# Kernel tuning notes

Measured on AMD Instinct MI355X. Metric: run time of the kernel, lower is better.

Reference implementation:

```python
import jax, jax.numpy as jnp
import numpy as np

K = 30           # SortPooling k (init kwarg)
B = 8192         # number of graphs in batch
MAX_N = 96       # max nodes per graph (sizes lie in [32, 96])
D = 128          # total_dim (feature width)


def _make_spans():
    # Ragged graph sizes in [32, 96], built in complementary pairs (a, 128-a)
    # so the total node count is exactly B * 64.
    i = np.arange(B // 2)
    a = 32 + (i * 7919) % 65          # in [32, 96]
    sizes = np.empty(B, dtype=np.int64)
    sizes[0::2] = a
    sizes[1::2] = 128 - a
    ends = np.cumsum(sizes)
    starts = ends - sizes
    return np.stack([starts, ends], axis=1)  # [B, 2]


def setup_inputs() -> dict:
    key = jax.random.key(0)
    spans = _make_spans()
    n_total = int(spans[-1, 1])  # 524288
    features = jax.random.normal(key, (n_total, D), dtype=jnp.float32)
    graph_indexes = jnp.asarray(spans, dtype=jnp.int64)
    return {"features": features, "graph_indexes": graph_indexes}


def reference(features, graph_indexes):
    n_total = features.shape[0]
    starts = graph_indexes[:, 0]                      # [B]
    ends = graph_indexes[:, 1]                        # [B]
    # Dense window per graph: indices start..start+MAX_N, masked past the end.
    idx = starts[:, None] + jnp.arange(MAX_N, dtype=graph_indexes.dtype)[None, :]  # [B, MAX_N]
    valid = idx < ends[:, None]                       # [B, MAX_N]
    g = features[jnp.minimum(idx, n_total - 1)]       # [B, MAX_N, D]
    # Sort key = last feature column; invalid slots -> -inf so they lose.
    sort_key = jnp.where(valid, g[:, :, -1], -jnp.inf)  # [B, MAX_N]
    _, top_idx = jax.lax.top_k(sort_key, K)           # [B, K] (stable ties, like tf.nn.top_k)
    rows = jnp.take_along_axis(g, top_idx[:, :, None], axis=1)      # [B, K, D]
    sel_valid = jnp.take_along_axis(valid, top_idx, axis=1)         # [B, K]
    # Graphs smaller than K get zero-padded rows (matches tf.concat with zeros).
    return jnp.where(sel_valid[:, :, None], rows, jnp.float32(0.0))
```

## Files before the change

### kernel.cpp

```cpp
#include <hip/hip_runtime.h>


#define KSEL   30
#define MAXN   96
#define DIM    128
#define BLOCK  256

__global__ __launch_bounds__(BLOCK) void sortpool_kernel(
    const float* __restrict__ feat,
    const int*   __restrict__ gi,
    float*       __restrict__ out)
{
    const int b = blockIdx.x;
    const int t = threadIdx.x;

    __shared__ float key[MAXN];
    __shared__ int   sel[KSEL];

    const int start = gi[2 * b];
    const int end   = gi[2 * b + 1];
    int n = end - start;
    if (n > MAXN) n = MAXN;

    if (t < KSEL) sel[t] = -1;
    if (t < n)
        key[t] = feat[(size_t)(start + t) * DIM + (DIM - 1)];
    __syncthreads();

    if (t < n) {
        const float ki = key[t];
        int rank = 0;
        #pragma unroll 4
        for (int j = 0; j < n; ++j) {
            const float kj = key[j];
            rank += (kj > ki) || (kj == ki && j < t);
        }
        if (rank < KSEL) sel[rank] = t;
    }
    __syncthreads();

    const size_t out_base = (size_t)b * (KSEL * DIM);
    for (int e = t; e < KSEL * (DIM / 4); e += BLOCK) {
        const int k = e >> 5;
        const int c = (e & 31) << 2;
        const int r = sel[k];
        float4 v;
        if (r >= 0) {
            v = *(const float4*)&feat[(size_t)(start + r) * DIM + c];
        } else {
            v = make_float4(0.f, 0.f, 0.f, 0.f);
        }
        *(float4*)&out[out_base + (size_t)k * DIM + c] = v;
    }
}

extern "C" void kernel_launch(void* const* d_in, const int* in_sizes, int n_in,
                              void* d_out, int out_size, void* d_ws, size_t ws_size,
                              hipStream_t stream) {
    const float* feat = (const float*)d_in[0];
    const int*   gi   = (const int*)d_in[1];
    float*       out  = (float*)d_out;

    const int B = in_sizes[1] / 2;
    sortpool_kernel<<<dim3(B), dim3(BLOCK), 0, stream>>>(feat, gi, out);
}
```

Baseline: 372.9 us.

## Process one graph per wavefront with wave-level barriers and nontemporal stores

Remaps the kernel so each 64-lane wavefront handles one graph, with four graphs per block instead of one graph per 256-thread block. Each lane ranks two nodes, and block-wide __syncthreads are replaced with wave barriers, which removes cross-wave synchronisation and idle threads during the rank phase. Output rows are written with nontemporal stores to avoid polluting cache. The trade-off is that each graph's gather and copy is done by only 64 lanes, so each wave carries more serial work, and stores that bypass the cache could behave differently.

```diff
diff --git a/kernel.cpp b/kernel.cpp
--- a/kernel.cpp
+++ b/kernel.cpp
@@ -4,53 +4,68 @@
 #define KSEL   30
 #define MAXN   96
 #define DIM    128
-#define BLOCK  256
+#define WPB    4
+#define BLOCK  (WPB * 64)
+
+typedef float f32x4 __attribute__((ext_vector_type(4)));
 
 __global__ __launch_bounds__(BLOCK) void sortpool_kernel(
     const float* __restrict__ feat,
     const int*   __restrict__ gi,
-    float*       __restrict__ out)
+    float*       __restrict__ out,
+    const int    nb)
 {
-    const int b = blockIdx.x;
-    const int t = threadIdx.x;
+    __shared__ float key[WPB][MAXN];
+    __shared__ int   sel[WPB][KSEL];
 
-    __shared__ float key[MAXN];
-    __shared__ int   sel[KSEL];
+    const int t = (int)threadIdx.x;
+    const int w = __builtin_amdgcn_readfirstlane(t >> 6);
+    const int L = t & 63;
+    const int b = (int)blockIdx.x * WPB + w;
+    if (b >= nb) return;
 
     const int start = gi[2 * b];
     const int end   = gi[2 * b + 1];
     int n = end - start;
     if (n > MAXN) n = MAXN;
 
-    if (t < KSEL) sel[t] = -1;
-    if (t < n)
-        key[t] = feat[(size_t)(start + t) * DIM + (DIM - 1)];
-    __syncthreads();
+    if (L < KSEL) sel[w][L] = -1;
 
-    if (t < n) {
-        const float ki = key[t];
-        int rank = 0;
-        #pragma unroll 4
-        for (int j = 0; j < n; ++j) {
-            const float kj = key[j];
-            rank += (kj > ki) || (kj == ki && j < t);
-        }
-        if (rank < KSEL) sel[rank] = t;
+    const bool v0 = (L < n);
+    const bool v1 = (L + 64 < n);
+    float k0 = 0.f, k1 = 0.f;
+    if (v0) {
+        k0 = feat[(size_t)(start + L) * DIM + (DIM - 1)];
+        key[w][L] = k0;
     }
-    __syncthreads();
+    if (v1) {
+        k1 = feat[(size_t)(start + L + 64) * DIM + (DIM - 1)];
+        key[w][L + 64] = k1;
+    }
+    __builtin_amdgcn_wave_barrier();
+
+    int r0 = 0, r1 = 0;
+    #pragma unroll 4
+    for (int j = 0; j < n; ++j) {
+        const float kj = key[w][j];
+        r0 += (int)((kj > k0) | ((kj == k0) & (j < L)));
+        r1 += (int)((kj > k1) | ((kj == k1) & (j < L + 64)));
+    }
+    if (v0 && r0 < KSEL) sel[w][r0] = L;
+    if (v1 && r1 < KSEL) sel[w][r1] = L + 64;
+    __builtin_amdgcn_wave_barrier();
 
     const size_t out_base = (size_t)b * (KSEL * DIM);
-    for (int e = t; e < KSEL * (DIM / 4); e += BLOCK) {
+    #pragma unroll 5
+    for (int i = 0; i < (KSEL * (DIM / 4)) / 64; ++i) {
+        const int e = i * 64 + L;
         const int k = e >> 5;
         const int c = (e & 31) << 2;
-        const int r = sel[k];
-        float4 v;
-        if (r >= 0) {
-            v = *(const float4*)&feat[(size_t)(start + r) * DIM + c];
-        } else {
-            v = make_float4(0.f, 0.f, 0.f, 0.f);
-        }
-        *(float4*)&out[out_base + (size_t)k * DIM + c] = v;
+        const int r = sel[w][k];
+        f32x4 v = (f32x4)(0.f);
+        if (r >= 0)
+            v = *(const f32x4*)&feat[(size_t)(start + r) * DIM + c];
+        __builtin_nontemporal_store(v, (f32x4*)&out[out_base + (size_t)k * DIM + c]);
     }
 }
 
@@ -62,5 +77,6 @@
     float*       out  = (float*)d_out;
 
     const int B = in_sizes[1] / 2;
-    sortpool_kernel<<<dim3(B), dim3(BLOCK), 0, stream>>>(feat, gi, out);
+    const int grid = (B + WPB - 1) / WPB;
+    sortpool_kernel<<<dim3(grid), dim3(BLOCK), 0, stream>>>(feat, gi, out, B);
 }
```

After: 386.1 us. 1.04x slower.
